# Kernel optimization log

Hardware: AMD Instinct MI355X
Metric: run time of the kernel (lower is better)

The kernel has to match this reference:

```python
import jax, jax.numpy as jnp
import numpy as np

B, C, H, W = 8, 16, 128, 128
P = H * W            # pixel_number = 16384
KN = 16              # kernel_number_per_pixel
CK = C * 9           # in_channel * kernel_size = 144


def setup_inputs() -> dict:
    key = jax.random.key(0)
    k1, k2, k3 = jax.random.split(key, 3)
    x = jax.random.normal(k1, (B, C, H, W), dtype=jnp.float32)
    weights = jax.random.normal(k2, (P, KN, CK), dtype=jnp.float32)
    hash_idx = jax.random.randint(k3, (P, CK), 0, C * H * W, dtype=jnp.int64)
    return {"x": x, "weights": weights, "hash_idx": hash_idx}


def reference(x, weights, hash_idx):
    b, c, h, w = x.shape
    img_size = c * h * w
    flat = x.reshape(-1)  # [B*C*H*W]
    # per-batch offset of the per-pixel hash table (torch fallback branch)
    idx = hash_idx[None, :, :] + (jnp.arange(b, dtype=hash_idx.dtype) * img_size)[:, None, None]  # [B,P,CK]
    patches = flat[idx]  # [B, P, CK] hash-indexed gather (im2col)
    # weights [P,KN,CK] @ patches [P,CK,B] -> [P,KN,B]; transpose(0,2) -> [B,KN,P]
    return jnp.einsum('pkc,bpc->bkp', weights, patches)
```

## Files before the change

kernel.cpp:

```cpp
#include <hip/hip_runtime.h>
#include <hip/hip_bf16.h>

#define P_TOTAL 16384
#define KN      16
#define CK      144
#define BATCH   8
#define IMG     262144
#define PSTRIDE 12

__global__ __launch_bounds__(256) void transpose_x_bf16(
    const float* __restrict__ x, float4* __restrict__ xt)
{
    const int i = blockIdx.x * 256 + threadIdx.x;
    union { __hip_bfloat16 h[8]; float4 f4; } u;
#pragma unroll
    for (int b = 0; b < BATCH; ++b)
        u.h[b] = __float2bfloat16(x[(size_t)b * IMG + i]);
    xt[i] = u.f4;
}

template <bool USE_XT>
__global__ __launch_bounds__(256) void abc2d_kernel(
    const void*  __restrict__ xsrc,
    const float* __restrict__ w,
    const int*   __restrict__ hidx,
    float* __restrict__ out)
{
    __shared__ float patch[CK * PSTRIDE];

    const int bid = blockIdx.x;
    const int p   = (bid & 7) * (P_TOTAL / 8) + (bid >> 3);
    const int t   = threadIdx.x;
    const int k   = t >> 4;
    const int cs  = t & 15;

    const float* wp = w + (size_t)p * (KN * CK) + (size_t)k * CK;
    float wreg[9];
#pragma unroll
    for (int i = 0; i < 9; ++i) wreg[i] = wp[cs + 16 * i];

    const int* hp = hidx + p * CK;
    if (USE_XT) {
        if (t < CK) {
            const int id = hp[t];
            union { __hip_bfloat16 h[8]; float4 f4; } u;
            u.f4 = reinterpret_cast<const float4*>(xsrc)[id];
            float* pr = &patch[t * PSTRIDE];
            *reinterpret_cast<float4*>(pr) = make_float4(
                __bfloat162float(u.h[0]), __bfloat162float(u.h[1]),
                __bfloat162float(u.h[2]), __bfloat162float(u.h[3]));
            *reinterpret_cast<float4*>(pr + 4) = make_float4(
                __bfloat162float(u.h[4]), __bfloat162float(u.h[5]),
                __bfloat162float(u.h[6]), __bfloat162float(u.h[7]));
        }
    } else {
        const float* xf = reinterpret_cast<const float*>(xsrc);
        for (int j = t; j < CK * BATCH; j += 256) {
            const int c = j >> 3;
            const int b = j & 7;
            patch[c * PSTRIDE + b] = xf[(size_t)hp[c] + (size_t)b * IMG];
        }
    }
    __syncthreads();

    float acc[BATCH];
#pragma unroll
    for (int b = 0; b < BATCH; ++b) acc[b] = 0.f;

#pragma unroll
    for (int i = 0; i < 9; ++i) {
        const int c = cs + 16 * i;
        const float wv = wreg[i];
        const float* pr = &patch[c * PSTRIDE];
        const float4 p0 = *reinterpret_cast<const float4*>(pr);
        const float4 p1 = *reinterpret_cast<const float4*>(pr + 4);
        acc[0] += wv * p0.x;
        acc[1] += wv * p0.y;
        acc[2] += wv * p0.z;
        acc[3] += wv * p0.w;
        acc[4] += wv * p1.x;
        acc[5] += wv * p1.y;
        acc[6] += wv * p1.z;
        acc[7] += wv * p1.w;
    }

#pragma unroll
    for (int b = 0; b < BATCH; ++b) {
        float v = acc[b];
        v += __shfl_xor(v, 1);
        v += __shfl_xor(v, 2);
        v += __shfl_xor(v, 4);
        v += __shfl_xor(v, 8);
        acc[b] = v;
    }

    if (cs == 0) {
#pragma unroll
        for (int b = 0; b < BATCH; ++b)
            out[(size_t)b * (KN * P_TOTAL) + (size_t)k * P_TOTAL + p] = acc[b];
    }
}

extern "C" void kernel_launch(void* const* d_in, const int* in_sizes, int n_in,
                              void* d_out, int out_size, void* d_ws, size_t ws_size,
                              hipStream_t stream) {
    const float* x    = (const float*)d_in[0];
    const float* wts  = (const float*)d_in[1];
    const int*   hidx = (const int*)d_in[2];
    float* out = (float*)d_out;

    const size_t xt_bytes = (size_t)IMG * BATCH * sizeof(__hip_bfloat16);
    if (ws_size >= xt_bytes) {
        float4* xt = (float4*)d_ws;
        transpose_x_bf16<<<IMG / 256, 256, 0, stream>>>(x, xt);
        abc2d_kernel<true><<<P_TOTAL, 256, 0, stream>>>((const void*)xt, wts, hidx, out);
    } else {
        abc2d_kernel<false><<<P_TOTAL, 256, 0, stream>>>((const void*)x, wts, hidx, out);
    }
}
```

Measured before the change: 239.3 us.

## Compute per-pixel GEMV with bf16 MFMA, one wave per pixel

Replaces the scalar FMA plus shuffle reduction with a 16x16x32 bf16 MFMA per wave, with each wave handling one pixel and four pixels per block. Each wave writes its gathered patch transposed into its own LDS region, so no block barrier is needed. Weights are converted to bf16 on the fly. This cuts instruction and synchronization overhead, but adds bf16 rounding of the weights and some wasted MFMA work on duplicated rows.

```diff
diff --git a/kernel.cpp b/kernel.cpp
--- a/kernel.cpp
+++ b/kernel.cpp
@@ -6,99 +6,131 @@
 #define CK      144
 #define BATCH   8
 #define IMG     262144
-#define PSTRIDE 12
+#define RWH     176
+
+typedef __attribute__((ext_vector_type(8))) short bf16x8;
+typedef __attribute__((ext_vector_type(4))) float f32x4;
+
+__device__ __forceinline__ short f2bf(float f) {
+    __hip_bfloat16 h = __float2bfloat16(f);
+    return *reinterpret_cast<short*>(&h);
+}
 
 __global__ __launch_bounds__(256) void transpose_x_bf16(
     const float* __restrict__ x, float4* __restrict__ xt)
 {
     const int i = blockIdx.x * 256 + threadIdx.x;
-    union { __hip_bfloat16 h[8]; float4 f4; } u;
+    union { short h[8]; float4 f4; } u;
 #pragma unroll
     for (int b = 0; b < BATCH; ++b)
-        u.h[b] = __float2bfloat16(x[(size_t)b * IMG + i]);
+        u.h[b] = f2bf(x[(size_t)b * IMG + i]);
     xt[i] = u.f4;
 }
 
-template <bool USE_XT>
-__global__ __launch_bounds__(256) void abc2d_kernel(
-    const void*  __restrict__ xsrc,
-    const float* __restrict__ w,
-    const int*   __restrict__ hidx,
+__global__ __launch_bounds__(256) void abc2d_mfma(
+    const float4* __restrict__ xt,
+    const float*  __restrict__ w,
+    const int*    __restrict__ hidx,
     float* __restrict__ out)
 {
-    __shared__ float patch[CK * PSTRIDE];
+    __shared__ short patchT[4 * 8 * RWH];
 
+    const int t    = threadIdx.x;
+    const int wv   = t >> 6;
+    const int lane = t & 63;
+    const int bid  = blockIdx.x;
+    const int p = (bid & 7) * (P_TOTAL / 8) + (bid >> 3) * 4 + wv;
+
+    short* pT = patchT + wv * 8 * RWH;
+
+    const int* hp = hidx + p * CK;
+    const int c0 = lane, c1 = lane + 64;
+    const int id0 = hp[c0];
+    const int id1 = hp[c1];
+    int id2 = 0;
+    if (lane < 16) id2 = hp[lane + 128];
+    union { short h[8]; float4 f4; } u0, u1, u2;
+    u0.f4 = xt[id0];
+    u1.f4 = xt[id1];
+    if (lane < 16) u2.f4 = xt[id2];
+#pragma unroll
+    for (int b = 0; b < BATCH; ++b) pT[b * RWH + c0] = u0.h[b];
+#pragma unroll
+    for (int b = 0; b < BATCH; ++b) pT[b * RWH + c1] = u1.h[b];
+    if (lane < 16) {
+#pragma unroll
+        for (int b = 0; b < BATCH; ++b) pT[b * RWH + lane + 128] = u2.h[b];
+    }
+    reinterpret_cast<int*>(pT)[(lane >> 3) * 88 + 72 + (lane & 7)] = 0;
+
+    const int n    = lane & 15;
+    const int q    = lane >> 4;
+    const int arow = n & 7;
+    const short* aptr = pT + arow * RWH;
+    const float* wp   = w + (size_t)p * (KN * CK) + (size_t)n * CK;
+
+    f32x4 acc = {0.f, 0.f, 0.f, 0.f};
+#pragma unroll
+    for (int s = 0; s < 5; ++s) {
+        const int c = 32 * s + 8 * q;
+        bf16x8 a = *reinterpret_cast<const bf16x8*>(aptr + c);
+        bf16x8 b = {0, 0, 0, 0, 0, 0, 0, 0};
+        if (c < CK) {
+            const float4 f0 = *reinterpret_cast<const float4*>(wp + c);
+            const float4 f1 = *reinterpret_cast<const float4*>(wp + c + 4);
+            b[0] = f2bf(f0.x); b[1] = f2bf(f0.y); b[2] = f2bf(f0.z); b[3] = f2bf(f0.w);
+            b[4] = f2bf(f1.x); b[5] = f2bf(f1.y); b[6] = f2bf(f1.z); b[7] = f2bf(f1.w);
+        }
+        acc = __builtin_amdgcn_mfma_f32_16x16x32_bf16(a, b, acc, 0, 0, 0);
+    }
+
+    if (lane < 32) {
+#pragma unroll
+        for (int i = 0; i < 4; ++i) {
+            const int b = q * 4 + i;
+            out[(size_t)b * (KN * P_TOTAL) + (size_t)n * P_TOTAL + p] = acc[i];
+        }
+    }
+}
+
+__global__ __launch_bounds__(256) void abc2d_fallback(
+    const float* __restrict__ x, const float* __restrict__ w,
+    const int* __restrict__ hidx, float* __restrict__ out)
+{
+    __shared__ float patch[CK * 12];
     const int bid = blockIdx.x;
     const int p   = (bid & 7) * (P_TOTAL / 8) + (bid >> 3);
     const int t   = threadIdx.x;
-    const int k   = t >> 4;
-    const int cs  = t & 15;
-
-    const float* wp = w + (size_t)p * (KN * CK) + (size_t)k * CK;
-    float wreg[9];
-#pragma unroll
-    for (int i = 0; i < 9; ++i) wreg[i] = wp[cs + 16 * i];
-
     const int* hp = hidx + p * CK;
-    if (USE_XT) {
-        if (t < CK) {
-            const int id = hp[t];
-            union { __hip_bfloat16 h[8]; float4 f4; } u;
-            u.f4 = reinterpret_cast<const float4*>(xsrc)[id];
-            float* pr = &patch[t * PSTRIDE];
-            *reinterpret_cast<float4*>(pr) = make_float4(
-                __bfloat162float(u.h[0]), __bfloat162float(u.h[1]),
-                __bfloat162float(u.h[2]), __bfloat162float(u.h[3]));
-            *reinterpret_cast<float4*>(pr + 4) = make_float4(
-                __bfloat162float(u.h[4]), __bfloat162float(u.h[5]),
-                __bfloat162float(u.h[6]), __bfloat162float(u.h[7]));
-        }
-    } else {
-        const float* xf = reinterpret_cast<const float*>(xsrc);
-        for (int j = t; j < CK * BATCH; j += 256) {
-            const int c = j >> 3;
-            const int b = j & 7;
-            patch[c * PSTRIDE + b] = xf[(size_t)hp[c] + (size_t)b * IMG];
-        }
+    for (int j = t; j < CK * BATCH; j += 256) {
+        const int c = j >> 3, b = j & 7;
+        patch[c * 12 + b] = x[(size_t)hp[c] + (size_t)b * IMG];
     }
     __syncthreads();
-
+    const int k = t >> 4, cs = t & 15;
+    const float* wp = w + (size_t)p * (KN * CK) + (size_t)k * CK;
     float acc[BATCH];
 #pragma unroll
     for (int b = 0; b < BATCH; ++b) acc[b] = 0.f;
-
 #pragma unroll
     for (int i = 0; i < 9; ++i) {
         const int c = cs + 16 * i;
-        const float wv = wreg[i];
-        const float* pr = &patch[c * PSTRIDE];
-        const float4 p0 = *reinterpret_cast<const float4*>(pr);
-        const float4 p1 = *reinterpret_cast<const float4*>(pr + 4);
-        acc[0] += wv * p0.x;
-        acc[1] += wv * p0.y;
-        acc[2] += wv * p0.z;
-        acc[3] += wv * p0.w;
-        acc[4] += wv * p1.x;
-        acc[5] += wv * p1.y;
-        acc[6] += wv * p1.z;
-        acc[7] += wv * p1.w;
+        const float wv = wp[c];
+        const float* pr = &patch[c * 12];
+#pragma unroll
+        for (int b = 0; b < BATCH; ++b) acc[b] += wv * pr[b];
     }
-
 #pragma unroll
     for (int b = 0; b < BATCH; ++b) {
         float v = acc[b];
-        v += __shfl_xor(v, 1);
-        v += __shfl_xor(v, 2);
-        v += __shfl_xor(v, 4);
-        v += __shfl_xor(v, 8);
+        v += __shfl_xor(v, 1); v += __shfl_xor(v, 2);
+        v += __shfl_xor(v, 4); v += __shfl_xor(v, 8);
         acc[b] = v;
     }
-
-    if (cs == 0) {
+    if (cs == 0)
 #pragma unroll
         for (int b = 0; b < BATCH; ++b)
             out[(size_t)b * (KN * P_TOTAL) + (size_t)k * P_TOTAL + p] = acc[b];
-    }
 }
 
 extern "C" void kernel_launch(void* const* d_in, const int* in_sizes, int n_in,
@@ -109,12 +141,12 @@
     const int*   hidx = (const int*)d_in[2];
     float* out = (float*)d_out;
 
-    const size_t xt_bytes = (size_t)IMG * BATCH * sizeof(__hip_bfloat16);
+    const size_t xt_bytes = (size_t)IMG * BATCH * sizeof(short);
     if (ws_size >= xt_bytes) {
         float4* xt = (float4*)d_ws;
         transpose_x_bf16<<<IMG / 256, 256, 0, stream>>>(x, xt);
-        abc2d_kernel<true><<<P_TOTAL, 256, 0, stream>>>((const void*)xt, wts, hidx, out);
+        abc2d_mfma<<<P_TOTAL / 4, 256, 0, stream>>>(xt, wts, hidx, out);
     } else {
-        abc2d_kernel<false><<<P_TOTAL, 256, 0, stream>>>((const void*)x, wts, hidx, out);
+        abc2d_fallback<<<P_TOTAL, 256, 0, stream>>>(x, wts, hidx, out);
     }
 }
```

Measured after the change: 241.4 us. About the same (+0.9%).
